# Kernel optimization log

Hardware: AMD Instinct MI355X
Metric: run time of the kernel (lower is better)

Reference implementation:

```python
import jax, jax.numpy as jnp
import numpy as np

D = 1024
NUM_HEADS = 16
HEAD_DIM = D // NUM_HEADS
INIT_VALUES = 1e-4


def setup_inputs() -> dict:
    key = jax.random.key(0)
    ks = jax.random.split(key, 24)
    s = 0.02
    inp = {
        "v": jax.random.normal(ks[0], (8, 2048, D), dtype=jnp.float32),
        "l": jax.random.normal(ks[1], (8, 512, D), dtype=jnp.float32),
        "ln_v_g": jnp.ones((D,), jnp.float32),
        "ln_v_b": jnp.zeros((D,), jnp.float32),
        "ln_l_g": jnp.ones((D,), jnp.float32),
        "ln_l_b": jnp.zeros((D,), jnp.float32),
        "gamma_v": jnp.full((D,), INIT_VALUES, jnp.float32),
        "gamma_l": jnp.full((D,), INIT_VALUES, jnp.float32),
    }
    names = ["Wq_v2l", "Wk_v2l", "Wv_v2l", "Wo_v2l", "Wq_l2v", "Wk_l2v", "Wv_l2v", "Wo_l2v"]
    for i, n in enumerate(names):
        inp[n] = jax.random.normal(ks[2 + i], (D, D), dtype=jnp.float32) * s
        inp[n.replace("W", "b")] = jnp.zeros((D,), jnp.float32)
    return inp


def layer_norm(x, g, b, eps=1e-5):
    mu = jnp.mean(x, axis=-1, keepdims=True)
    var = jnp.var(x, axis=-1, keepdims=True)
    return (x - mu) * jax.lax.rsqrt(var + eps) * g + b


def mha(q_in, k_in, v_in, Wq, bq, Wk, bk, Wv, bv, Wo, bo):
    B, Sq, _ = q_in.shape
    Sk = k_in.shape[1]
    # torch Linear: x @ W.T + b
    q = (q_in @ Wq.T + bq).reshape(B, Sq, NUM_HEADS, HEAD_DIM)
    k = (k_in @ Wk.T + bk).reshape(B, Sk, NUM_HEADS, HEAD_DIM)
    v = (v_in @ Wv.T + bv).reshape(B, Sk, NUM_HEADS, HEAD_DIM)
    scores = jnp.einsum("bqhd,bkhd->bhqk", q, k) / np.sqrt(HEAD_DIM).astype(np.float32)
    attn = jax.nn.softmax(scores, axis=-1)
    ctx = jnp.einsum("bhqk,bkhd->bqhd", attn, v).reshape(B, Sq, D)
    return ctx @ Wo.T + bo


def reference(v, l, ln_v_g, ln_v_b, ln_l_g, ln_l_b, gamma_v, gamma_l,
              Wq_v2l, bq_v2l, Wk_v2l, bk_v2l, Wv_v2l, bv_v2l, Wo_v2l, bo_v2l,
              Wq_l2v, bq_l2v, Wk_l2v, bk_l2v, Wv_l2v, bv_l2v, Wo_l2v, bo_l2v):
    # eval mode: dropout and drop_path are identity
    v_norm = layer_norm(v, ln_v_g, ln_v_b)
    l_norm = layer_norm(l, ln_l_g, ln_l_b)
    updated_v = mha(v_norm, l_norm, l_norm,
                    Wq_v2l, bq_v2l, Wk_v2l, bk_v2l, Wv_v2l, bv_v2l, Wo_v2l, bo_v2l)
    updated_l = mha(l_norm, v_norm, v_norm,
                    Wq_l2v, bq_l2v, Wk_l2v, bk_l2v, Wv_l2v, bv_l2v, Wo_l2v, bo_l2v)
    v_out = v + gamma_v * updated_v
    l_out = l + gamma_l * updated_l
    return (v_out, l_out)
```

## Files before the change

kernel.cpp:

```cpp
#include <hip/hip_runtime.h>
#include <hip/hip_bf16.h>
#include <stdint.h>

typedef __bf16 bf16x8 __attribute__((ext_vector_type(8)));
typedef float f32x4 __attribute__((ext_vector_type(4)));
typedef float f32x16 __attribute__((ext_vector_type(16)));
typedef uint32_t u32x4 __attribute__((ext_vector_type(4)));
typedef unsigned short u16;

typedef __attribute__((address_space(1))) void as1_void;
typedef __attribute__((address_space(3))) void as3_void;

#define BAR() __builtin_amdgcn_s_barrier()
#define VMCNT(n) asm volatile("s_waitcnt vmcnt(" #n ")" ::: "memory")
#define LGKM0() asm volatile("s_waitcnt lgkmcnt(0)" ::: "memory")

__device__ __forceinline__ u16 f2bf(float f) {
  uint32_t u = __float_as_uint(f);
  u += 0x7fffu + ((u >> 16) & 1u);
  return (u16)(u >> 16);
}

struct Seg {
  const u16* W;
  const float* bias;
  u16* outb;
  float* outf;
  const float* res;
  const float* gamma;
  int mode;
  int sk;
  float ascale;
};

__global__ __launch_bounds__(256) void cvt8_kernel(
    const float4* s0, const float4* s1, const float4* s2, const float4* s3,
    const float4* s4, const float4* s5, const float4* s6, const float4* s7,
    ushort4* d0, ushort4* d1, ushort4* d2, ushort4* d3,
    ushort4* d4, ushort4* d5, ushort4* d6, ushort4* d7) {
  const float4* s; ushort4* d;
  switch (blockIdx.y) {
    case 0: s = s0; d = d0; break;
    case 1: s = s1; d = d1; break;
    case 2: s = s2; d = d2; break;
    case 3: s = s3; d = d3; break;
    case 4: s = s4; d = d4; break;
    case 5: s = s5; d = d5; break;
    case 6: s = s6; d = d6; break;
    default: s = s7; d = d7; break;
  }
  int i = blockIdx.x * 256 + threadIdx.x;
  float4 v = s[i];
  ushort4 o;
  o.x = f2bf(v.x); o.y = f2bf(v.y); o.z = f2bf(v.z); o.w = f2bf(v.w);
  d[i] = o;
}

__global__ __launch_bounds__(256) void ln_kernel(const float* __restrict__ x,
                                                 const float* __restrict__ g,
                                                 const float* __restrict__ b,
                                                 u16* __restrict__ out) {
  int row = blockIdx.x;
  int t = threadIdx.x;
  const float4* xr = (const float4*)(x + (size_t)row * 1024);
  float4 v = xr[t];
  float s = v.x + v.y + v.z + v.w;
  float s2 = v.x * v.x + v.y * v.y + v.z * v.z + v.w * v.w;
#pragma unroll
  for (int off = 1; off < 64; off <<= 1) {
    s += __shfl_xor(s, off);
    s2 += __shfl_xor(s2, off);
  }
  __shared__ float red[8];
  int wv = t >> 6;
  if ((t & 63) == 0) { red[wv] = s; red[4 + wv] = s2; }
  __syncthreads();
  s = red[0] + red[1] + red[2] + red[3];
  s2 = red[4] + red[5] + red[6] + red[7];
  float mu = s * (1.0f / 1024.0f);
  float var = s2 * (1.0f / 1024.0f) - mu * mu;
  float rstd = rsqrtf(var + 1e-5f);
  const float4 gv = ((const float4*)g)[t];
  const float4 bv = ((const float4*)b)[t];
  ushort4 o;
  o.x = f2bf((v.x - mu) * rstd * gv.x + bv.x);
  o.y = f2bf((v.y - mu) * rstd * gv.y + bv.y);
  o.z = f2bf((v.z - mu) * rstd * gv.z + bv.z);
  o.w = f2bf((v.w - mu) * rstd * gv.w + bv.w);
  ((ushort4*)out)[(size_t)row * 256 + t] = o;
}

__global__ __launch_bounds__(256, 3) void gemm_v7(
    const u16* __restrict__ A, Seg s0, Seg s1, Seg s2,
    int mtiles, int ntiles) {
  const int K = 1024;
  int hwid = blockIdx.x;
  int xcd = hwid & 7, q = hwid >> 3;
  int mchunk = mtiles >> 3;
  int mt = xcd * mchunk + q / ntiles;
  int nt = q % ntiles;
  int m0 = mt * 128;
  int si = nt >> 3;
  Seg seg = (si == 0) ? s0 : (si == 1) ? s1 : s2;
  int nl0 = (nt & 7) * 128;

  int t = threadIdx.x, lane = t & 63, wv = t >> 6;
  int wr = wv >> 1, wc = wv & 1;
  int lr = lane & 15, lg = lane >> 4;

  __shared__ u16 SA[3][128 * 32];
  __shared__ u16 SB[3][128 * 32];

  int row0 = t >> 2, c0 = t & 3;
  int sco = (c0 ^ (row0 & 3)) * 8;
  const u16* gA0 = A + (size_t)(m0 + row0) * K + sco;
  const u16* gB0 = seg.W + (size_t)(nl0 + row0) * K + sco;

  auto STAGE = [&](int slot, int kt) {
    __builtin_amdgcn_global_load_lds((const as1_void*)(gA0 + kt * 32),
                                     (as3_void*)(&SA[slot][0] + t * 8), 16, 0, 0);
    __builtin_amdgcn_global_load_lds((const as1_void*)(gA0 + (size_t)64 * K + kt * 32),
                                     (as3_void*)(&SA[slot][0] + 2048 + t * 8), 16, 0, 0);
    __builtin_amdgcn_global_load_lds((const as1_void*)(gB0 + kt * 32),
                                     (as3_void*)(&SB[slot][0] + t * 8), 16, 0, 0);
    __builtin_amdgcn_global_load_lds((const as1_void*)(gB0 + (size_t)64 * K + kt * 32),
                                     (as3_void*)(&SB[slot][0] + 2048 + t * 8), 16, 0, 0);
  };

  f32x4 acc[4][4] = {};

  STAGE(0, 0); STAGE(1, 1); STAGE(2, 2);
  VMCNT(8);
  BAR();

  int slot = 0;
  const int NKT = K / 32;
#pragma unroll 1
  for (int kt = 0; kt < NKT; ++kt) {
    bf16x8 aX[4], bX[4];
#pragma unroll
    for (int m = 0; m < 4; ++m) {
      int row = wr * 64 + m * 16 + lr;
      aX[m] = *(const bf16x8*)(&SA[slot][0] + row * 32 + ((lg ^ (row & 3)) * 8));
    }
#pragma unroll
    for (int n = 0; n < 4; ++n) {
      int row = wc * 64 + n * 16 + lr;
      bX[n] = *(const bf16x8*)(&SB[slot][0] + row * 32 + ((lg ^ (row & 3)) * 8));
    }
    LGKM0();
    BAR();
    if (kt + 3 < NKT) STAGE(slot, kt + 3);
    __builtin_amdgcn_s_setprio(1);
#pragma unroll
    for (int m = 0; m < 4; ++m)
#pragma unroll
      for (int n = 0; n < 4; ++n)
        acc[m][n] = __builtin_amdgcn_mfma_f32_16x16x32_bf16(aX[m], bX[n], acc[m][n], 0, 0, 0);
    __builtin_amdgcn_s_setprio(0);
    if (kt + 3 < NKT) { VMCNT(8); }
    else if (kt + 3 == NKT) { VMCNT(4); }
    else if (kt + 2 == NKT) { VMCNT(0); }
    BAR();
    slot = (slot == 2) ? 0 : slot + 1;
  }

  int rowb = m0 + wr * 64 + (lane >> 4) * 4;
#pragma unroll
  for (int m = 0; m < 4; ++m) {
#pragma unroll
    for (int n = 0; n < 4; ++n) {
      int scol = nl0 + wc * 64 + n * 16 + lr;
      float bcol = seg.bias[scol];
#pragma unroll
      for (int r = 0; r < 4; ++r) {
        int row = rowb + m * 16 + r;
        float val = (acc[m][n][r] + bcol) * seg.ascale;
        if (seg.mode == 0) {
          seg.outb[(size_t)row * 1024 + scol] = f2bf(val);
        } else if (seg.mode == 1) {
          size_t idx = (size_t)row * 1024 + scol;
          seg.outf[idx] = seg.res[idx] + seg.gamma[scol] * val;
        } else {
          int bb = row >> seg.sk;
          int ss = row & ((1 << seg.sk) - 1);
          int h = scol >> 6, d = scol & 63;
          seg.outb[((((size_t)bb * 16 + h) * 64 + d) << seg.sk) + ss] = f2bf(val);
        }
      }
    }
  }
}

__global__ __launch_bounds__(256, 4) void attn_kernel(
    const u16* __restrict__ Q, const u16* __restrict__ Kmat,
    const u16* __restrict__ Vt, u16* __restrict__ ctx,
    int Sq, int Sk, int nq_shift) {
  int f = blockIdx.x;
  int xcd = f & 7, slot = f >> 3;
  int group = xcd * 16 + (slot >> nq_shift);
  int qt = slot & ((1 << nq_shift) - 1);
  int b = group >> 4, h = group & 15;
  int t = threadIdx.x, lane = t & 63, wv = t >> 6;
  int l31 = lane & 31, hi = lane >> 5;

  __shared__ u16 Ks[2][64 * 64];
  __shared__ u16 Vs[2][64 * 64];

  int q0 = qt * 128 + wv * 32;
  const u16* Qb = Q + (size_t)(b * Sq + q0 + l31) * 1024 + h * 64 + hi * 8;
  bf16x8 qf[4];
#pragma unroll
  for (int ds = 0; ds < 4; ++ds) qf[ds] = *(const bf16x8*)(Qb + ds * 16);

  int trow = t >> 3, tc = t & 7;
  int sc = (tc ^ (trow & 7)) * 8;
  const u16* gk = Kmat + (size_t)(b * Sk + trow) * 1024 + h * 64 + sc;
  const u16* gv = Vt + (size_t)((b * 16 + h) * 64 + trow) * Sk + sc;

  auto STAGE = [&](int buf, int kt) {
    const u16* k0 = gk + (size_t)(kt * 64) * 1024;
    const u16* v0 = gv + kt * 64;
    __builtin_amdgcn_global_load_lds((const as1_void*)k0, (as3_void*)(Ks[buf] + t * 8), 16, 0, 0);
    __builtin_amdgcn_global_load_lds((const as1_void*)(k0 + (size_t)32 * 1024), (as3_void*)(Ks[buf] + 2048 + t * 8), 16, 0, 0);
    __builtin_amdgcn_global_load_lds((const as1_void*)v0, (as3_void*)(Vs[buf] + t * 8), 16, 0, 0);
    __builtin_amdgcn_global_load_lds((const as1_void*)(v0 + (size_t)32 * Sk), (as3_void*)(Vs[buf] + 2048 + t * 8), 16, 0, 0);
  };

  STAGE(0, 0);
  __syncthreads();

  f32x16 acc0 = {}, acc1 = {};
  float m_run = -1e30f, l_run = 0.f;
  int sw = l31 & 7;

  int nt = Sk >> 6;
  for (int kt = 0; kt < nt; ++kt) {
    int cur = kt & 1;
    if (kt + 1 < nt) STAGE(cur ^ 1, kt + 1);
    const u16* kb = Ks[cur];
    f32x16 s0v = {}, s1v = {};
    __builtin_amdgcn_s_setprio(1);
#pragma unroll
    for (int ds = 0; ds < 4; ++ds) {
      int blk = 2 * ds + hi;
      bf16x8 ka0 = *(const bf16x8*)(kb + l31 * 64 + ((blk ^ sw) * 8));
      bf16x8 ka1 = *(const bf16x8*)(kb + (32 + l31) * 64 + ((blk ^ sw) * 8));
      s0v = __builtin_amdgcn_mfma_f32_32x32x16_bf16(ka0, qf[ds], s0v, 0, 0, 0);
      s1v = __builtin_amdgcn_mfma_f32_32x32x16_bf16(ka1, qf[ds], s1v, 0, 0, 0);
    }
    __builtin_amdgcn_s_setprio(0);
    float mx = s0v[0];
#pragma unroll
    for (int i = 1; i < 16; ++i) mx = fmaxf(mx, s0v[i]);
#pragma unroll
    for (int i = 0; i < 16; ++i) mx = fmaxf(mx, s1v[i]);
    mx = fmaxf(mx, __shfl_xor(mx, 32));
    if (__any(mx > m_run + 8.f)) {
      float mnew = fmaxf(m_run, mx);
      float fac = __builtin_amdgcn_exp2f(m_run - mnew);
#pragma unroll
      for (int r = 0; r < 16; ++r) {
        int src = (r & 3) + 8 * (r >> 2) + 4 * hi;
        float fr = __shfl(fac, src);
        acc0[r] *= fr;
        acc1[r] *= fr;
      }
      l_run *= fac;
      m_run = mnew;
    }
    float sum = 0.f;
#pragma unroll
    for (int i = 0; i < 16; ++i) {
      s0v[i] = __builtin_amdgcn_exp2f(s0v[i] - m_run);
      sum += s0v[i];
    }
#pragma unroll
    for (int i = 0; i < 16; ++i) {
      s1v[i] = __builtin_amdgcn_exp2f(s1v[i] - m_run);
      sum += s1v[i];
    }
    sum += __shfl_xor(sum, 32);
    l_run += sum;
    bf16x8 pa[4];
#pragma unroll
    for (int g = 0; g < 2; ++g) {
      const f32x16& s = g ? s1v : s0v;
#pragma unroll
      for (int half = 0; half < 2; ++half) {
        int o = half * 8;
        uint32_t a0, a1, b0, b1;
        asm("v_cvt_pk_bf16_f32 %0, %1, %2" : "=v"(a0) : "v"(s[o + 0]), "v"(s[o + 1]));
        asm("v_cvt_pk_bf16_f32 %0, %1, %2" : "=v"(a1) : "v"(s[o + 2]), "v"(s[o + 3]));
        asm("v_cvt_pk_bf16_f32 %0, %1, %2" : "=v"(b0) : "v"(s[o + 4]), "v"(s[o + 5]));
        asm("v_cvt_pk_bf16_f32 %0, %1, %2" : "=v"(b1) : "v"(s[o + 6]), "v"(s[o + 7]));
        asm("v_permlane32_swap_b32 %0, %1" : "+v"(a0), "+v"(b0));
        asm("v_permlane32_swap_b32 %0, %1" : "+v"(a1), "+v"(b1));
        u32x4 w;
        w[0] = a0; w[1] = a1; w[2] = b0; w[3] = b1;
        pa[g * 2 + half] = __builtin_bit_cast(bf16x8, w);
      }
    }
    const u16* vb = Vs[cur];
    __builtin_amdgcn_s_setprio(1);
#pragma unroll
    for (int ks = 0; ks < 4; ++ks) {
      int blk = 2 * ks + hi;
      bf16x8 vf0 = *(const bf16x8*)(vb + l31 * 64 + ((blk ^ sw) * 8));
      bf16x8 vf1 = *(const bf16x8*)(vb + (32 + l31) * 64 + ((blk ^ sw) * 8));
      acc0 = __builtin_amdgcn_mfma_f32_32x32x16_bf16(pa[ks], vf0, acc0, 0, 0, 0);
      acc1 = __builtin_amdgcn_mfma_f32_32x32x16_bf16(pa[ks], vf1, acc1, 0, 0, 0);
    }
    __builtin_amdgcn_s_setprio(0);
    __syncthreads();
  }
  float linv = 1.0f / l_run;
  u16* cb = ctx + (size_t)(b * Sq + q0) * 1024 + h * 64;
#pragma unroll
  for (int r = 0; r < 16; ++r) {
    int src = (r & 3) + 8 * (r >> 2) + 4 * hi;
    float li = __shfl(linv, src);
    cb[(size_t)src * 1024 + l31] = f2bf(acc0[r] * li);
    cb[(size_t)src * 1024 + 32 + l31] = f2bf(acc1[r] * li);
  }
}

extern "C" void kernel_launch(void* const* d_in, const int* in_sizes, int n_in,
                              void* d_out, int out_size, void* d_ws, size_t ws_size,
                              hipStream_t stream) {
  const float* v = (const float*)d_in[0];
  const float* l = (const float*)d_in[1];
  const float* ln_v_g = (const float*)d_in[2];
  const float* ln_v_b = (const float*)d_in[3];
  const float* ln_l_g = (const float*)d_in[4];
  const float* ln_l_b = (const float*)d_in[5];
  const float* gamma_v = (const float*)d_in[6];
  const float* gamma_l = (const float*)d_in[7];
  const float* Wf[8];
  const float* Bf[8];
  for (int i = 0; i < 8; ++i) {
    Wf[i] = (const float*)d_in[8 + 2 * i];
    Bf[i] = (const float*)d_in[9 + 2 * i];
  }
  float* v_out = (float*)d_out;
  float* l_out = v_out + (size_t)16384 * 1024;

  char* p = (char*)d_ws;
  auto alloc = [&](size_t bytes) {
    char* r = p;
    p += (bytes + 255) & ~(size_t)255;
    return r;
  };
  u16* Wbf[8];
  for (int i = 0; i < 8; ++i) Wbf[i] = (u16*)alloc((size_t)1024 * 1024 * 2);
  u16* vn   = (u16*)alloc((size_t)16384 * 1024 * 2);
  u16* lnm  = (u16*)alloc((size_t)4096 * 1024 * 2);
  u16* bufA = (u16*)alloc((size_t)16384 * 1024 * 2);
  u16* bufB = (u16*)alloc((size_t)4096 * 1024 * 2);
  u16* bufC = (u16*)alloc((size_t)4096 * 1024 * 2);
  u16* bufD = (u16*)alloc((size_t)16384 * 1024 * 2);
  u16* bufF = (u16*)alloc((size_t)4096 * 1024 * 2);

  const float QSC = 0.125f * 1.4426950408889634f;
  Seg zs = {};

  cvt8_kernel<<<dim3(1024, 8), 256, 0, stream>>>(
      (const float4*)Wf[0], (const float4*)Wf[1], (const float4*)Wf[2], (const float4*)Wf[3],
      (const float4*)Wf[4], (const float4*)Wf[5], (const float4*)Wf[6], (const float4*)Wf[7],
      (ushort4*)Wbf[0], (ushort4*)Wbf[1], (ushort4*)Wbf[2], (ushort4*)Wbf[3],
      (ushort4*)Wbf[4], (ushort4*)Wbf[5], (ushort4*)Wbf[6], (ushort4*)Wbf[7]);
  ln_kernel<<<16384, 256, 0, stream>>>(v, ln_v_g, ln_v_b, vn);
  ln_kernel<<<4096, 256, 0, stream>>>(l, ln_l_g, ln_l_b, lnm);

  {
    Seg a = {Wbf[4], Bf[4], bufB, nullptr, nullptr, nullptr, 0, 0, QSC};
    Seg b = {Wbf[1], Bf[1], bufF, nullptr, nullptr, nullptr, 0, 0, 1.0f};
    Seg c = {Wbf[2], Bf[2], bufC, nullptr, nullptr, nullptr, 2, 9, 1.0f};
    gemm_v7<<<dim3(768), 256, 0, stream>>>(lnm, a, b, c, 32, 24);
  }
  {
    Seg q = {Wbf[0], Bf[0], bufA, nullptr, nullptr, nullptr, 0, 0, QSC};
    gemm_v7<<<dim3(1024), 256, 0, stream>>>(vn, q, zs, zs, 128, 8);
  }
  attn_kernel<<<dim3(2048), 256, 0, stream>>>(bufA, bufF, bufC, bufA, 2048, 512, 4);
  {
    Seg o = {Wbf[3], Bf[3], nullptr, v_out, v, gamma_v, 1, 0, 1.0f};
    gemm_v7<<<dim3(1024), 256, 0, stream>>>(bufA, o, zs, zs, 128, 8);
  }
  {
    Seg k = {Wbf[5], Bf[5], bufA, nullptr, nullptr, nullptr, 0, 0, 1.0f};
    Seg vv = {Wbf[6], Bf[6], bufD, nullptr, nullptr, nullptr, 2, 11, 1.0f};
    gemm_v7<<<dim3(2048), 256, 0, stream>>>(vn, k, vv, zs, 128, 16);
  }
  attn_kernel<<<dim3(512), 256, 0, stream>>>(bufB, bufA, bufD, bufB, 512, 2048, 2);
  {
    Seg o = {Wbf[7], Bf[7], nullptr, l_out, l, gamma_l, 1, 0, 1.0f};
    gemm_v7<<<dim3(256), 256, 0, stream>>>(bufB, o, zs, zs, 32, 8);
  }
}
```

Measured before the change: 506.3 us.

## Fuse Q/K/V projections of v, retune LDS swizzle, vectorize transposed epilogue

Merges the v-side Q projection with the l2v K and V projections into one 3072-block GEMM launch that reads vn once. K now goes into a new buffer (bufG), because bufA still holds Q. The LDS XOR swizzle now keys on (row>>1)&3 instead of row&3 to change the bank-conflict pattern. The mode-2 transposed-V epilogue writes four consecutive bf16 values as one ushort4 instead of four scalar stores. The mode-1 path drops the ascale multiply and mode 2 ignores ascale. All affected segments use ascale 1.0, and the change adds another 32 MB workspace buffer.

After: 479.6 us. 1.06x faster.

```diff
diff --git a/kernel.cpp b/kernel.cpp
--- a/kernel.cpp
+++ b/kernel.cpp
@@ -112,7 +112,7 @@
   __shared__ u16 SB[3][128 * 32];
 
   int row0 = t >> 2, c0 = t & 3;
-  int sco = (c0 ^ (row0 & 3)) * 8;
+  int sco = (c0 ^ ((row0 >> 1) & 3)) * 8;
   const u16* gA0 = A + (size_t)(m0 + row0) * K + sco;
   const u16* gB0 = seg.W + (size_t)(nl0 + row0) * K + sco;
 
@@ -141,12 +141,12 @@
 #pragma unroll
     for (int m = 0; m < 4; ++m) {
       int row = wr * 64 + m * 16 + lr;
-      aX[m] = *(const bf16x8*)(&SA[slot][0] + row * 32 + ((lg ^ (row & 3)) * 8));
+      aX[m] = *(const bf16x8*)(&SA[slot][0] + row * 32 + ((lg ^ ((row >> 1) & 3)) * 8));
     }
 #pragma unroll
     for (int n = 0; n < 4; ++n) {
       int row = wc * 64 + n * 16 + lr;
-      bX[n] = *(const bf16x8*)(&SB[slot][0] + row * 32 + ((lg ^ (row & 3)) * 8));
+      bX[n] = *(const bf16x8*)(&SB[slot][0] + row * 32 + ((lg ^ ((row >> 1) & 3)) * 8));
     }
     LGKM0();
     BAR();
@@ -172,20 +172,26 @@
     for (int n = 0; n < 4; ++n) {
       int scol = nl0 + wc * 64 + n * 16 + lr;
       float bcol = seg.bias[scol];
-#pragma unroll
-      for (int r = 0; r < 4; ++r) {
-        int row = rowb + m * 16 + r;
-        float val = (acc[m][n][r] + bcol) * seg.ascale;
-        if (seg.mode == 0) {
-          seg.outb[(size_t)row * 1024 + scol] = f2bf(val);
-        } else if (seg.mode == 1) {
-          size_t idx = (size_t)row * 1024 + scol;
-          seg.outf[idx] = seg.res[idx] + seg.gamma[scol] * val;
-        } else {
-          int bb = row >> seg.sk;
-          int ss = row & ((1 << seg.sk) - 1);
-          int h = scol >> 6, d = scol & 63;
-          seg.outb[((((size_t)bb * 16 + h) * 64 + d) << seg.sk) + ss] = f2bf(val);
+      int row = rowb + m * 16;
+      if (seg.mode == 2) {
+        int bb = row >> seg.sk;
+        int ss = row & ((1 << seg.sk) - 1);
+        int h = scol >> 6, d = scol & 63;
+        ushort4 o;
+        o.x = f2bf(acc[m][n][0] + bcol);
+        o.y = f2bf(acc[m][n][1] + bcol);
+        o.z = f2bf(acc[m][n][2] + bcol);
+        o.w = f2bf(acc[m][n][3] + bcol);
+        *(ushort4*)(seg.outb + ((((size_t)bb * 16 + h) * 64 + d) << seg.sk) + ss) = o;
+      } else if (seg.mode == 0) {
+#pragma unroll
+        for (int r = 0; r < 4; ++r)
+          seg.outb[(size_t)(row + r) * 1024 + scol] = f2bf((acc[m][n][r] + bcol) * seg.ascale);
+      } else {
+#pragma unroll
+        for (int r = 0; r < 4; ++r) {
+          size_t idx = (size_t)(row + r) * 1024 + scol;
+          seg.outf[idx] = seg.res[idx] + seg.gamma[scol] * (acc[m][n][r] + bcol);
         }
       }
     }
@@ -360,6 +366,7 @@
   u16* bufC = (u16*)alloc((size_t)4096 * 1024 * 2);
   u16* bufD = (u16*)alloc((size_t)16384 * 1024 * 2);
   u16* bufF = (u16*)alloc((size_t)4096 * 1024 * 2);
+  u16* bufG = (u16*)alloc((size_t)16384 * 1024 * 2);
 
   const float QSC = 0.125f * 1.4426950408889634f;
   Seg zs = {};
@@ -380,19 +387,16 @@
   }
   {
     Seg q = {Wbf[0], Bf[0], bufA, nullptr, nullptr, nullptr, 0, 0, QSC};
-    gemm_v7<<<dim3(1024), 256, 0, stream>>>(vn, q, zs, zs, 128, 8);
+    Seg k = {Wbf[5], Bf[5], bufG, nullptr, nullptr, nullptr, 0, 0, 1.0f};
+    Seg vv = {Wbf[6], Bf[6], bufD, nullptr, nullptr, nullptr, 2, 11, 1.0f};
+    gemm_v7<<<dim3(3072), 256, 0, stream>>>(vn, q, k, vv, 128, 24);
   }
   attn_kernel<<<dim3(2048), 256, 0, stream>>>(bufA, bufF, bufC, bufA, 2048, 512, 4);
   {
     Seg o = {Wbf[3], Bf[3], nullptr, v_out, v, gamma_v, 1, 0, 1.0f};
     gemm_v7<<<dim3(1024), 256, 0, stream>>>(bufA, o, zs, zs, 128, 8);
   }
-  {
-    Seg k = {Wbf[5], Bf[5], bufA, nullptr, nullptr, nullptr, 0, 0, 1.0f};
-    Seg vv = {Wbf[6], Bf[6], bufD, nullptr, nullptr, nullptr, 2, 11, 1.0f};
-    gemm_v7<<<dim3(2048), 256, 0, stream>>>(vn, k, vv, zs, 128, 16);
-  }
-  attn_kernel<<<dim3(512), 256, 0, stream>>>(bufB, bufA, bufD, bufB, 512, 2048, 2);
+  attn_kernel<<<dim3(512), 256, 0, stream>>>(bufB, bufG, bufD, bufB, 512, 2048, 2);
   {
     Seg o = {Wbf[7], Bf[7], nullptr, l_out, l, gamma_l, 1, 0, 1.0f};
     gemm_v7<<<dim3(256), 256, 0, stream>>>(bufB, o, zs, zs, 32, 8);
```
